# Performance work log

Measured on AMD Instinct MI355X. Metric: run time of the kernel, lower is better.

The kernel has to match this reference:

```python
import jax, jax.numpy as jnp
import numpy as np

KNOTS = 16
BOUND = 5.0
BATCH = 500000
X_DIM = 6          # split into lower(3) / upper(3)
C_DIM = 4
HID = 128
SPLINE_DIM = 3 * KNOTS - 1   # 47 (non-periodic)
LOWER = X_DIM // 2
OUT_DIM = LOWER * SPLINE_DIM


def setup_inputs() -> dict:
    key = jax.random.key(0)
    ks = jax.random.split(key, 10)
    def glorot(k, shape):
        fan_in, fan_out = shape
        s = jnp.sqrt(2.0 / (fan_in + fan_out))
        return (jax.random.normal(k, shape, jnp.float32) * s)
    return {
        "x": jax.random.normal(ks[0], (BATCH, X_DIM), jnp.float32),
        "c": jax.random.normal(ks[1], (BATCH, C_DIM), jnp.float32),
        "W1": glorot(ks[2], (LOWER + C_DIM + 0 + (X_DIM - LOWER), HID))[: X_DIM - LOWER + C_DIM],
        "b1": jnp.zeros((HID,), jnp.float32),
        "W2": glorot(ks[3], (HID, HID)),
        "b2": jnp.zeros((HID,), jnp.float32),
        "W3": glorot(ks[4], (HID, OUT_DIM)),
        "b3": jnp.zeros((OUT_DIM,), jnp.float32),
        "train": False,
    }


def _mlp(h, W1, b1, W2, b2, W3, b3):
    h = jax.nn.relu(h @ W1 + b1)
    h = jax.nn.relu(h @ W2 + b2)
    return h @ W3 + b3


def _rqs_forward(x, W, H, D, B):
    """Rational-quadratic spline (Durkan et al.) forward.
    x: [N,d]; W,H: [N,d,K] bin widths/heights; D: [N,d,K-1] interior derivs."""
    K = W.shape[-1]
    pad = jnp.full(W.shape[:-1] + (1,), -B, W.dtype)
    xk = jnp.concatenate([pad, -B + jnp.cumsum(W, axis=-1)], axis=-1)  # [N,d,K+1]
    yk = jnp.concatenate([pad, -B + jnp.cumsum(H, axis=-1)], axis=-1)
    one = jnp.ones(D.shape[:-1] + (1,), D.dtype)
    dk = jnp.concatenate([one, D, one], axis=-1)                        # [N,d,K+1]

    oob = (x <= -B) | (x >= B)
    xm = jnp.where(oob, -B, x)
    # bin index per element (searchsorted via comparison-sum)
    idx = jnp.clip(jnp.sum((xm[..., None] >= xk), axis=-1) - 1, 0, K - 1)[..., None]

    gat = lambda a, i: jnp.take_along_axis(a, i, axis=-1)[..., 0]
    xk_b = gat(xk, idx)
    yk_b = gat(yk, idx)
    wk = gat(xk, idx + 1) - xk_b
    hk = gat(yk, idx + 1) - yk_b
    dk_b = gat(dk, idx)
    dk1 = gat(dk, idx + 1)

    sk = hk / wk
    relx = jnp.clip((xm - xk_b) / wk, 0.0, 1.0)
    r1 = relx * (1.0 - relx)
    den = sk + (dk1 + dk_b - 2.0 * sk) * r1
    num = hk * (sk * relx * relx + dk_b * r1)
    y = yk_b + num / den
    ld = (2.0 * jnp.log(sk)
          + jnp.log(dk1 * relx * relx + 2.0 * sk * r1 + dk_b * (1.0 - relx) ** 2)
          - 2.0 * jnp.log(den))

    y = jnp.where(oob, x, y)
    ld = jnp.where(oob, 0.0, ld)
    return y, jnp.sum(ld, axis=1)


def reference(x, c, W1, b1, W2, b2, W3, b3, train):
    lower, upper = x[:, :LOWER], x[:, LOWER:]
    h = jnp.hstack((upper, c))
    p = _mlp(h, W1, b1, W2, b2, W3, b3)
    p = p.reshape(-1, LOWER, SPLINE_DIM)
    Wb, Hb, Db = jnp.split(p, [KNOTS, 2 * KNOTS], axis=2)
    Wb = 2.0 * BOUND * jax.nn.softmax(Wb, axis=-1)
    Hb = 2.0 * BOUND * jax.nn.softmax(Hb, axis=-1)
    Db = jax.nn.softplus(Db)
    lo_t, log_det = _rqs_forward(lower, Wb, Hb, Db, BOUND)
    y = jnp.hstack((lo_t, upper))
    return y, log_det
```

## Files before the change

### kernel.cpp

```cpp
#include <hip/hip_runtime.h>
#include <math.h>


#define TILE 128
#define NT   256
#define HID  128
#define OUTD 141
#define HS   136
#define PRS  48
#define SRS  152
#define BND  5.0f
#define T1   0.5413248546f

typedef __bf16 bf16;
typedef _Float16 f16;
typedef __attribute__((ext_vector_type(8))) __bf16 bf16x8;
typedef __attribute__((ext_vector_type(8))) _Float16 f16x8;
typedef __attribute__((ext_vector_type(4))) float f32x4;

#define W1P_ELEMS (8 * 64 * 8)
#define W2P_ELEMS (8 * 4 * 64 * 8)
#define W3P_ELEMS (9 * 4 * 64 * 8)

#define SMEM_BYTES 40448

__global__ void nsc_prepack(const float* __restrict__ W1, const float* __restrict__ W2,
                            const float* __restrict__ W3,
                            bf16* __restrict__ W1p, bf16* __restrict__ W2p,
                            bf16* __restrict__ W3p) {
    int f = blockIdx.x * 256 + threadIdx.x;
    int lane = f & 63, lm = lane & 15, lq = lane >> 4;
    if (f < 512) {
        int t = f >> 6;
        int n = t * 16 + lm;
        bf16x8 pk;
        #pragma unroll
        for (int j = 0; j < 8; ++j) {
            int k = lq * 8 + j;
            pk[j] = (k < 7) ? (bf16)W1[k * HID + n] : (bf16)0.f;
        }
        *(bf16x8*)&W1p[(size_t)f * 8] = pk;
    } else if (f < 512 + 2048) {
        int g2 = f - 512;
        int tk = g2 >> 6, t = tk >> 2, ks = tk & 3;
        int n = t * 16 + lm;
        bf16x8 pk;
        #pragma unroll
        for (int j = 0; j < 8; ++j) {
            int p = ks * 32 + lq * 8 + j;
            int k = ((p & 7) << 4) | (p >> 3);
            pk[j] = (bf16)W2[k * HID + n];
        }
        *(bf16x8*)&W2p[(size_t)g2 * 8] = pk;
    } else if (f < 512 + 2048 + 2304) {
        int g3 = f - 2560;
        int tk = g3 >> 6, t = tk >> 2, ks = tk & 3;
        int col = t * 16 + lm;
        bf16x8 pk;
        #pragma unroll
        for (int j = 0; j < 8; ++j) {
            int p = ks * 32 + lq * 8 + j;
            int k = ((p & 7) << 4) | (p >> 3);
            pk[j] = (col < OUTD) ? (bf16)W3[k * OUTD + col] : (bf16)0.f;
        }
        *(bf16x8*)&W3p[(size_t)g3 * 8] = pk;
    }
}

__global__ __launch_bounds__(NT, 4) void nsc_main(
    const float* __restrict__ x, const float* __restrict__ c,
    const bf16* __restrict__ W1p, const float* __restrict__ b1,
    const bf16* __restrict__ W2p, const float* __restrict__ b2,
    const bf16* __restrict__ W3p, const float* __restrict__ b3,
    float* __restrict__ out_y, float* __restrict__ out_ld, int N)
{
    __shared__ __align__(16) char smem[SMEM_BYTES];
    bf16*  hbuf  = (bf16*)smem;
    f16*   shp16 = (f16*)smem;
    float* shld  = (float*)(smem + 38912);

    const int tid  = threadIdx.x;
    const int g0   = blockIdx.x * TILE;
    const int lane = tid & 63;
    const int wv   = tid >> 6;
    const int lm   = lane & 15;
    const int lq   = lane >> 4;
    const int sbase = wv * 32;
    const int arow0 = sbase + lm;
    const int arow1 = sbase + 16 + lm;

    if (lane < 32) {
        int s = sbase + lane;
        int g = g0 + s;
        float v[7];
        if (g < N) {
            v[0] = x[g * 6 + 3]; v[1] = x[g * 6 + 4]; v[2] = x[g * 6 + 5];
            v[3] = c[g * 4];     v[4] = c[g * 4 + 1];
            v[5] = c[g * 4 + 2]; v[6] = c[g * 4 + 3];
        } else {
            #pragma unroll
            for (int k = 0; k < 7; ++k) v[k] = 0.f;
        }
        bf16x8 r0 = (bf16x8){(bf16)v[0], (bf16)v[1], (bf16)v[2], (bf16)v[3],
                             (bf16)v[4], (bf16)v[5], (bf16)v[6], (bf16)0.f};
        bf16x8 z  = (bf16x8){(bf16)0.f, (bf16)0.f, (bf16)0.f, (bf16)0.f,
                             (bf16)0.f, (bf16)0.f, (bf16)0.f, (bf16)0.f};
        *(bf16x8*)&hbuf[s * HS]      = r0;
        *(bf16x8*)&hbuf[s * HS + 8]  = z;
        *(bf16x8*)&hbuf[s * HS + 16] = z;
        *(bf16x8*)&hbuf[s * HS + 24] = z;
    }

    {
        f32x4 acc1[2][8];
        #pragma unroll
        for (int t = 0; t < 8; ++t) {
            float b = b1[t * 16 + lm];
            acc1[0][t] = (f32x4){b, b, b, b};
            acc1[1][t] = (f32x4){b, b, b, b};
        }
        bf16x8 a0 = *(const bf16x8*)&hbuf[arow0 * HS + lq * 8];
        bf16x8 a1 = *(const bf16x8*)&hbuf[arow1 * HS + lq * 8];
        #pragma unroll
        for (int t = 0; t < 8; ++t) {
            bf16x8 bf = *(const bf16x8*)&W1p[(size_t)(t * 64 + lane) * 8];
            acc1[0][t] = __builtin_amdgcn_mfma_f32_16x16x32_bf16(a0, bf, acc1[0][t], 0, 0, 0);
            acc1[1][t] = __builtin_amdgcn_mfma_f32_16x16x32_bf16(a1, bf, acc1[1][t], 0, 0, 0);
        }
        #pragma unroll
        for (int ar = 0; ar < 2; ++ar)
            #pragma unroll
            for (int r = 0; r < 4; ++r) {
                bf16x8 pk;
                #pragma unroll
                for (int t = 0; t < 8; ++t) pk[t] = (bf16)fmaxf(acc1[ar][t][r], 0.f);
                int s = sbase + ar * 16 + lq * 4 + r;
                *(bf16x8*)&hbuf[s * HS + lm * 8] = pk;
            }
    }

    {
        f32x4 acc2[2][8];
        #pragma unroll
        for (int t = 0; t < 8; ++t) {
            float b = b2[t * 16 + lm];
            acc2[0][t] = (f32x4){b, b, b, b};
            acc2[1][t] = (f32x4){b, b, b, b};
        }
        #pragma unroll
        for (int ks = 0; ks < 4; ++ks) {
            bf16x8 a0 = *(const bf16x8*)&hbuf[arow0 * HS + ks * 32 + lq * 8];
            bf16x8 a1 = *(const bf16x8*)&hbuf[arow1 * HS + ks * 32 + lq * 8];
            #pragma unroll
            for (int t = 0; t < 8; ++t) {
                bf16x8 bf = *(const bf16x8*)&W2p[(size_t)((t * 4 + ks) * 64 + lane) * 8];
                acc2[0][t] = __builtin_amdgcn_mfma_f32_16x16x32_bf16(a0, bf, acc2[0][t], 0, 0, 0);
                acc2[1][t] = __builtin_amdgcn_mfma_f32_16x16x32_bf16(a1, bf, acc2[1][t], 0, 0, 0);
            }
        }
        #pragma unroll
        for (int ar = 0; ar < 2; ++ar)
            #pragma unroll
            for (int r = 0; r < 4; ++r) {
                bf16x8 pk;
                #pragma unroll
                for (int t = 0; t < 8; ++t) pk[t] = (bf16)fmaxf(acc2[ar][t][r], 0.f);
                int s = sbase + ar * 16 + lq * 4 + r;
                *(bf16x8*)&hbuf[s * HS + lm * 8] = pk;
            }
    }

    f32x4 acc3[2][9];
    {
        #pragma unroll
        for (int t = 0; t < 9; ++t) {
            int col = t * 16 + lm;
            float b = (col < OUTD) ? b3[col] : 0.f;
            acc3[0][t] = (f32x4){b, b, b, b};
            acc3[1][t] = (f32x4){b, b, b, b};
        }
        #pragma unroll
        for (int ks = 0; ks < 4; ++ks) {
            bf16x8 a0 = *(const bf16x8*)&hbuf[arow0 * HS + ks * 32 + lq * 8];
            bf16x8 a1 = *(const bf16x8*)&hbuf[arow1 * HS + ks * 32 + lq * 8];
            #pragma unroll
            for (int t = 0; t < 9; ++t) {
                bf16x8 bf = *(const bf16x8*)&W3p[(size_t)((t * 4 + ks) * 64 + lane) * 8];
                acc3[0][t] = __builtin_amdgcn_mfma_f32_16x16x32_bf16(a0, bf, acc3[0][t], 0, 0, 0);
                acc3[1][t] = __builtin_amdgcn_mfma_f32_16x16x32_bf16(a1, bf, acc3[1][t], 0, 0, 0);
            }
        }
    }
    __syncthreads();

    #pragma unroll
    for (int t = 0; t < 9; ++t) {
        int col = t * 16 + lm;
        if (col < OUTD) {
            int d = (col >= 94) ? 2 : ((col >= 47) ? 1 : 0);
            int off = d * PRS + (col - d * 47);
            #pragma unroll
            for (int ar = 0; ar < 2; ++ar)
                #pragma unroll
                for (int r = 0; r < 4; ++r) {
                    int s = sbase + ar * 16 + lq * 4 + r;
                    shp16[s * SRS + off] = (f16)acc3[ar][t][r];
                }
        }
    }
    __syncthreads();

    for (int pidx = tid; pidx < TILE * 3; pidx += NT) {
        const int s = pidx / 3, d = pidx - s * 3;
        const int g = g0 + s;
        if (g < N) {
            const f16* pr = &shp16[s * SRS + d * PRS];
            f16x8 v0 = *(const f16x8*)&pr[0];
            f16x8 v1 = *(const f16x8*)&pr[8];
            f16x8 v2 = *(const f16x8*)&pr[16];
            f16x8 v3 = *(const f16x8*)&pr[24];
            f16x8 v4 = *(const f16x8*)&pr[32];
            f16x8 v5 = *(const f16x8*)&pr[40];
            float wv_[16], hv[16], dl[15];
            #pragma unroll
            for (int i = 0; i < 8; ++i) {
                wv_[i] = (float)v0[i]; wv_[8 + i] = (float)v1[i];
                hv[i]  = (float)v2[i]; hv[8 + i]  = (float)v3[i];
            }
            #pragma unroll
            for (int i = 0; i < 8; ++i) dl[i] = (float)v4[i];
            #pragma unroll
            for (int i = 0; i < 7; ++i) dl[8 + i] = (float)v5[i];

            float sw = 0.f, sh = 0.f;
            #pragma unroll
            for (int i = 0; i < 16; ++i) { wv_[i] = __expf(wv_[i]); sw += wv_[i]; }
            #pragma unroll
            for (int i = 0; i < 16; ++i) { hv[i]  = __expf(hv[i]);  sh += hv[i]; }
            float cwn = 10.f * __builtin_amdgcn_rcpf(sw);
            float chn = 10.f * __builtin_amdgcn_rcpf(sh);
            #pragma unroll
            for (int i = 0; i < 16; ++i) { wv_[i] *= cwn; hv[i] *= chn; }

            float xv = x[g * 6 + d];
            bool oob = (xv <= -BND) || (xv >= BND);
            float xm = oob ? -BND : xv;

            float cumx = -BND + wv_[0], cumy = -BND + hv[0];
            float xk_b = -BND, yk_b = -BND;
            float wk = wv_[0], hk = hv[0];
            float d0l = T1, d1l = dl[0];
            #pragma unroll
            for (int i = 1; i < 16; ++i) {
                bool ge = (xm >= cumx);
                if (ge) {
                    xk_b = cumx; yk_b = cumy;
                    wk = wv_[i]; hk = hv[i];
                    d0l = dl[i - 1];
                    d1l = (i < 15) ? dl[i] : T1;
                }
                cumx += wv_[i]; cumy += hv[i];
            }
            float d0 = (d0l > 15.f) ? d0l : __logf(1.f + __expf(d0l));
            float d1 = (d1l > 15.f) ? d1l : __logf(1.f + __expf(d1l));

            float rwk = __builtin_amdgcn_rcpf(wk);
            float sk = hk * rwk;
            float relx = (xm - xk_b) * rwk;
            relx = fminf(fmaxf(relx, 0.f), 1.f);
            float r1 = relx * (1.f - relx);
            float den = sk + (d1 + d0 - 2.f * sk) * r1;
            float iden = __builtin_amdgcn_rcpf(den);
            float num = hk * (sk * relx * relx + d0 * r1);
            float y = yk_b + num * iden;
            float omr = 1.f - relx;
            float arg = d1 * relx * relx + 2.f * sk * r1 + d0 * omr * omr;
            float ratio = sk * iden;
            float ld = __logf(ratio * ratio * arg);
            if (oob) { y = xv; ld = 0.f; }

            out_y[g * 6 + d] = y;
            out_y[g * 6 + 3 + d] = x[g * 6 + 3 + d];
            shld[s * 3 + d] = ld;
        }
    }
    __syncthreads();

    if (tid < TILE) {
        int g = g0 + tid;
        if (g < N)
            out_ld[g] = shld[tid * 3] + shld[tid * 3 + 1] + shld[tid * 3 + 2];
    }
}

extern "C" void kernel_launch(void* const* d_in, const int* in_sizes, int n_in,
                              void* d_out, int out_size, void* d_ws, size_t ws_size,
                              hipStream_t stream) {
    const float* x  = (const float*)d_in[0];
    const float* c  = (const float*)d_in[1];
    const float* W1 = (const float*)d_in[2];
    const float* b1 = (const float*)d_in[3];
    const float* W2 = (const float*)d_in[4];
    const float* b2 = (const float*)d_in[5];
    const float* W3 = (const float*)d_in[6];
    const float* b3 = (const float*)d_in[7];

    const int N = in_sizes[0] / 6;
    float* out_y  = (float*)d_out;
    float* out_ld = (float*)d_out + (size_t)N * 6;

    bf16* W1p = (bf16*)d_ws;
    bf16* W2p = W1p + W1P_ELEMS;
    bf16* W3p = W2p + W2P_ELEMS;

    int nfrag = 512 + 2048 + 2304;
    nsc_prepack<<<(nfrag + 255) / 256, 256, 0, stream>>>(W1, W2, W3, W1p, W2p, W3p);

    int nblocks = (N + TILE - 1) / TILE;
    nsc_main<<<nblocks, NT, 0, stream>>>(x, c, W1p, b1, W2p, b2, W3p, b3,
                                         out_y, out_ld, N);
}
```

Baseline: 159.1 us.

## Keep MLP activations in registers via transposed MFMA operand layout

Swaps the MFMA operand roles so the weights act as the A operand and the activations as B, with W2/W3 prepacked in a permuted feature order. The accumulator layout of one layer then feeds the next layer directly from registers, which removes the LDS round trips and syncs between MLP layers. Layer 2 and 3 are tiled so fewer accumulators are live at once, layer-3 outputs are written to LDS as packed f16x4 at contiguous offsets, and the spline stage assigns each wave one dimension with per-dimension unpacking. This adds register pressure from holding activation fragments and makes the spline loads unaligned for dimensions 1 and 2.

```diff
diff --git a/kernel.cpp b/kernel.cpp
--- a/kernel.cpp
+++ b/kernel.cpp
@@ -6,8 +6,6 @@
 #define NT   256
 #define HID  128
 #define OUTD 141
-#define HS   136
-#define PRS  48
 #define SRS  152
 #define BND  5.0f
 #define T1   0.5413248546f
@@ -16,54 +14,59 @@
 typedef _Float16 f16;
 typedef __attribute__((ext_vector_type(8))) __bf16 bf16x8;
 typedef __attribute__((ext_vector_type(8))) _Float16 f16x8;
+typedef __attribute__((ext_vector_type(4))) _Float16 f16x4;
+typedef __attribute__((ext_vector_type(2))) _Float16 f16x2;
 typedef __attribute__((ext_vector_type(4))) float f32x4;
 
 #define W1P_ELEMS (8 * 64 * 8)
 #define W2P_ELEMS (8 * 4 * 64 * 8)
 #define W3P_ELEMS (9 * 4 * 64 * 8)
+#define NFRAG (512 + 2048 + 2304)
+#define B3P_OFF ((W1P_ELEMS + W2P_ELEMS + W3P_ELEMS) * 2)
 
 #define SMEM_BYTES 40448
 
 __global__ void nsc_prepack(const float* __restrict__ W1, const float* __restrict__ W2,
-                            const float* __restrict__ W3,
+                            const float* __restrict__ W3, const float* __restrict__ b3,
                             bf16* __restrict__ W1p, bf16* __restrict__ W2p,
-                            bf16* __restrict__ W3p) {
+                            bf16* __restrict__ W3p, float* __restrict__ b3p) {
     int f = blockIdx.x * 256 + threadIdx.x;
     int lane = f & 63, lm = lane & 15, lq = lane >> 4;
     if (f < 512) {
         int t = f >> 6;
-        int n = t * 16 + lm;
+        int m = t * 16 + lm;
         bf16x8 pk;
         #pragma unroll
         for (int j = 0; j < 8; ++j) {
             int k = lq * 8 + j;
-            pk[j] = (k < 7) ? (bf16)W1[k * HID + n] : (bf16)0.f;
+            pk[j] = (k < 7) ? (bf16)W1[k * HID + m] : (bf16)0.f;
         }
         *(bf16x8*)&W1p[(size_t)f * 8] = pk;
     } else if (f < 512 + 2048) {
         int g2 = f - 512;
-        int tk = g2 >> 6, t = tk >> 2, ks = tk & 3;
-        int n = t * 16 + lm;
+        int tk = g2 >> 6, t2 = tk >> 2, kc = tk & 3;
+        int m = t2 * 16 + lm;
         bf16x8 pk;
         #pragma unroll
         for (int j = 0; j < 8; ++j) {
-            int p = ks * 32 + lq * 8 + j;
-            int k = ((p & 7) << 4) | (p >> 3);
-            pk[j] = (bf16)W2[k * HID + n];
+            int feat = ((kc * 2 + (j >> 2)) << 4) + (lq << 2) + (j & 3);
+            pk[j] = (bf16)W2[feat * HID + m];
         }
         *(bf16x8*)&W2p[(size_t)g2 * 8] = pk;
-    } else if (f < 512 + 2048 + 2304) {
+    } else if (f < NFRAG) {
         int g3 = f - 2560;
-        int tk = g3 >> 6, t = tk >> 2, ks = tk & 3;
-        int col = t * 16 + lm;
+        int tk = g3 >> 6, t3 = tk >> 2, kc = tk & 3;
+        int col = t3 * 16 + lm;
         bf16x8 pk;
         #pragma unroll
         for (int j = 0; j < 8; ++j) {
-            int p = ks * 32 + lq * 8 + j;
-            int k = ((p & 7) << 4) | (p >> 3);
-            pk[j] = (col < OUTD) ? (bf16)W3[k * OUTD + col] : (bf16)0.f;
+            int feat = ((kc * 2 + (j >> 2)) << 4) + (lq << 2) + (j & 3);
+            pk[j] = (col < OUTD) ? (bf16)W3[feat * OUTD + col] : (bf16)0.f;
         }
         *(bf16x8*)&W3p[(size_t)g3 * 8] = pk;
+    } else if (f < NFRAG + 144) {
+        int i = f - NFRAG;
+        b3p[i] = (i < OUTD) ? b3[i] : 0.f;
     }
 }
 
@@ -71,11 +74,10 @@
     const float* __restrict__ x, const float* __restrict__ c,
     const bf16* __restrict__ W1p, const float* __restrict__ b1,
     const bf16* __restrict__ W2p, const float* __restrict__ b2,
-    const bf16* __restrict__ W3p, const float* __restrict__ b3,
+    const bf16* __restrict__ W3p, const float* __restrict__ b3p,
     float* __restrict__ out_y, float* __restrict__ out_ld, int N)
 {
     __shared__ __align__(16) char smem[SMEM_BYTES];
-    bf16*  hbuf  = (bf16*)smem;
     f16*   shp16 = (f16*)smem;
     float* shld  = (float*)(smem + 38912);
 
@@ -86,180 +88,194 @@
     const int lm   = lane & 15;
     const int lq   = lane >> 4;
     const int sbase = wv * 32;
-    const int arow0 = sbase + lm;
-    const int arow1 = sbase + 16 + lm;
-
-    if (lane < 32) {
-        int s = sbase + lane;
-        int g = g0 + s;
-        float v[7];
-        if (g < N) {
+
+    bf16x8 inb[2];
+    #pragma unroll
+    for (int set = 0; set < 2; ++set) {
+        int g = g0 + sbase + set * 16 + lm;
+        float v[8] = {0.f, 0.f, 0.f, 0.f, 0.f, 0.f, 0.f, 0.f};
+        if (lq == 0 && g < N) {
             v[0] = x[g * 6 + 3]; v[1] = x[g * 6 + 4]; v[2] = x[g * 6 + 5];
             v[3] = c[g * 4];     v[4] = c[g * 4 + 1];
             v[5] = c[g * 4 + 2]; v[6] = c[g * 4 + 3];
-        } else {
-            #pragma unroll
-            for (int k = 0; k < 7; ++k) v[k] = 0.f;
-        }
-        bf16x8 r0 = (bf16x8){(bf16)v[0], (bf16)v[1], (bf16)v[2], (bf16)v[3],
-                             (bf16)v[4], (bf16)v[5], (bf16)v[6], (bf16)0.f};
-        bf16x8 z  = (bf16x8){(bf16)0.f, (bf16)0.f, (bf16)0.f, (bf16)0.f,
-                             (bf16)0.f, (bf16)0.f, (bf16)0.f, (bf16)0.f};
-        *(bf16x8*)&hbuf[s * HS]      = r0;
-        *(bf16x8*)&hbuf[s * HS + 8]  = z;
-        *(bf16x8*)&hbuf[s * HS + 16] = z;
-        *(bf16x8*)&hbuf[s * HS + 24] = z;
-    }
-
+        }
+        bf16x8 t;
+        #pragma unroll
+        for (int j = 0; j < 8; ++j) t[j] = (bf16)v[j];
+        inb[set] = t;
+    }
+
+    f32x4 acc1[2][8];
     {
-        f32x4 acc1[2][8];
         #pragma unroll
         for (int t = 0; t < 8; ++t) {
-            float b = b1[t * 16 + lm];
-            acc1[0][t] = (f32x4){b, b, b, b};
-            acc1[1][t] = (f32x4){b, b, b, b};
-        }
-        bf16x8 a0 = *(const bf16x8*)&hbuf[arow0 * HS + lq * 8];
-        bf16x8 a1 = *(const bf16x8*)&hbuf[arow1 * HS + lq * 8];
+            f32x4 bb = *(const f32x4*)&b1[t * 16 + lq * 4];
+            acc1[0][t] = bb; acc1[1][t] = bb;
+        }
         #pragma unroll
         for (int t = 0; t < 8; ++t) {
-            bf16x8 bf = *(const bf16x8*)&W1p[(size_t)(t * 64 + lane) * 8];
-            acc1[0][t] = __builtin_amdgcn_mfma_f32_16x16x32_bf16(a0, bf, acc1[0][t], 0, 0, 0);
-            acc1[1][t] = __builtin_amdgcn_mfma_f32_16x16x32_bf16(a1, bf, acc1[1][t], 0, 0, 0);
-        }
-        #pragma unroll
-        for (int ar = 0; ar < 2; ++ar)
-            #pragma unroll
-            for (int r = 0; r < 4; ++r) {
-                bf16x8 pk;
-                #pragma unroll
-                for (int t = 0; t < 8; ++t) pk[t] = (bf16)fmaxf(acc1[ar][t][r], 0.f);
-                int s = sbase + ar * 16 + lq * 4 + r;
-                *(bf16x8*)&hbuf[s * HS + lm * 8] = pk;
+            bf16x8 wf = *(const bf16x8*)&W1p[(size_t)(t * 64 + lane) * 8];
+            acc1[0][t] = __builtin_amdgcn_mfma_f32_16x16x32_bf16(wf, inb[0], acc1[0][t], 0, 0, 0);
+            acc1[1][t] = __builtin_amdgcn_mfma_f32_16x16x32_bf16(wf, inb[1], acc1[1][t], 0, 0, 0);
+        }
+    }
+    bf16x8 h1B[2][4];
+    #pragma unroll
+    for (int set = 0; set < 2; ++set)
+        #pragma unroll
+        for (int kc = 0; kc < 4; ++kc) {
+            bf16x8 hb;
+            #pragma unroll
+            for (int j = 0; j < 8; ++j)
+                hb[j] = (bf16)fmaxf(acc1[set][kc * 2 + (j >> 2)][j & 3], 0.f);
+            h1B[set][kc] = hb;
+        }
+
+    bf16x8 h2B[2][4];
+    #pragma unroll
+    for (int tp = 0; tp < 4; ++tp) {
+        f32x4 acc[2][2];
+        #pragma unroll
+        for (int dt = 0; dt < 2; ++dt) {
+            f32x4 bb = *(const f32x4*)&b2[(tp * 2 + dt) * 16 + lq * 4];
+            acc[0][dt] = bb; acc[1][dt] = bb;
+        }
+        #pragma unroll
+        for (int kc = 0; kc < 4; ++kc)
+            #pragma unroll
+            for (int dt = 0; dt < 2; ++dt) {
+                bf16x8 wf = *(const bf16x8*)&W2p[(size_t)(((tp * 2 + dt) * 4 + kc) * 64 + lane) * 8];
+                acc[0][dt] = __builtin_amdgcn_mfma_f32_16x16x32_bf16(wf, h1B[0][kc], acc[0][dt], 0, 0, 0);
+                acc[1][dt] = __builtin_amdgcn_mfma_f32_16x16x32_bf16(wf, h1B[1][kc], acc[1][dt], 0, 0, 0);
             }
-    }
-
-    {
-        f32x4 acc2[2][8];
-        #pragma unroll
-        for (int t = 0; t < 8; ++t) {
-            float b = b2[t * 16 + lm];
-            acc2[0][t] = (f32x4){b, b, b, b};
-            acc2[1][t] = (f32x4){b, b, b, b};
-        }
-        #pragma unroll
-        for (int ks = 0; ks < 4; ++ks) {
-            bf16x8 a0 = *(const bf16x8*)&hbuf[arow0 * HS + ks * 32 + lq * 8];
-            bf16x8 a1 = *(const bf16x8*)&hbuf[arow1 * HS + ks * 32 + lq * 8];
-            #pragma unroll
-            for (int t = 0; t < 8; ++t) {
-                bf16x8 bf = *(const bf16x8*)&W2p[(size_t)((t * 4 + ks) * 64 + lane) * 8];
-                acc2[0][t] = __builtin_amdgcn_mfma_f32_16x16x32_bf16(a0, bf, acc2[0][t], 0, 0, 0);
-                acc2[1][t] = __builtin_amdgcn_mfma_f32_16x16x32_bf16(a1, bf, acc2[1][t], 0, 0, 0);
+        #pragma unroll
+        for (int set = 0; set < 2; ++set) {
+            bf16x8 hb;
+            #pragma unroll
+            for (int j = 0; j < 8; ++j)
+                hb[j] = (bf16)fmaxf(acc[set][j >> 2][j & 3], 0.f);
+            h2B[set][tp] = hb;
+        }
+    }
+
+    #pragma unroll
+    for (int t3 = 0; t3 < 9; ++t3) {
+        f32x4 acc[2];
+        {
+            f32x4 bb = *(const f32x4*)&b3p[t3 * 16 + lq * 4];
+            acc[0] = bb; acc[1] = bb;
+        }
+        #pragma unroll
+        for (int kc = 0; kc < 4; ++kc) {
+            bf16x8 wf = *(const bf16x8*)&W3p[(size_t)((t3 * 4 + kc) * 64 + lane) * 8];
+            acc[0] = __builtin_amdgcn_mfma_f32_16x16x32_bf16(wf, h2B[0][kc], acc[0], 0, 0, 0);
+            acc[1] = __builtin_amdgcn_mfma_f32_16x16x32_bf16(wf, h2B[1][kc], acc[1], 0, 0, 0);
+        }
+        #pragma unroll
+        for (int set = 0; set < 2; ++set) {
+            int s = sbase + set * 16 + lm;
+            f16x4 pk = (f16x4){(f16)acc[set][0], (f16)acc[set][1],
+                               (f16)acc[set][2], (f16)acc[set][3]};
+            int off = t3 * 16 + lq * 4;
+            if (t3 < 8) {
+                *(f16x4*)&shp16[s * SRS + off] = pk;
+            } else {
+                if (lq < 3) *(f16x4*)&shp16[s * SRS + off] = pk;
+                else        shp16[s * SRS + 140] = pk[0];
             }
         }
-        #pragma unroll
-        for (int ar = 0; ar < 2; ++ar)
-            #pragma unroll
-            for (int r = 0; r < 4; ++r) {
-                bf16x8 pk;
-                #pragma unroll
-                for (int t = 0; t < 8; ++t) pk[t] = (bf16)fmaxf(acc2[ar][t][r], 0.f);
-                int s = sbase + ar * 16 + lq * 4 + r;
-                *(bf16x8*)&hbuf[s * HS + lm * 8] = pk;
-            }
-    }
-
-    f32x4 acc3[2][9];
-    {
-        #pragma unroll
-        for (int t = 0; t < 9; ++t) {
-            int col = t * 16 + lm;
-            float b = (col < OUTD) ? b3[col] : 0.f;
-            acc3[0][t] = (f32x4){b, b, b, b};
-            acc3[1][t] = (f32x4){b, b, b, b};
-        }
-        #pragma unroll
-        for (int ks = 0; ks < 4; ++ks) {
-            bf16x8 a0 = *(const bf16x8*)&hbuf[arow0 * HS + ks * 32 + lq * 8];
-            bf16x8 a1 = *(const bf16x8*)&hbuf[arow1 * HS + ks * 32 + lq * 8];
-            #pragma unroll
-            for (int t = 0; t < 9; ++t) {
-                bf16x8 bf = *(const bf16x8*)&W3p[(size_t)((t * 4 + ks) * 64 + lane) * 8];
-                acc3[0][t] = __builtin_amdgcn_mfma_f32_16x16x32_bf16(a0, bf, acc3[0][t], 0, 0, 0);
-                acc3[1][t] = __builtin_amdgcn_mfma_f32_16x16x32_bf16(a1, bf, acc3[1][t], 0, 0, 0);
-            }
-        }
     }
     __syncthreads();
 
-    #pragma unroll
-    for (int t = 0; t < 9; ++t) {
-        int col = t * 16 + lm;
-        if (col < OUTD) {
-            int d = (col >= 94) ? 2 : ((col >= 47) ? 1 : 0);
-            int off = d * PRS + (col - d * 47);
-            #pragma unroll
-            for (int ar = 0; ar < 2; ++ar)
-                #pragma unroll
-                for (int r = 0; r < 4; ++r) {
-                    int s = sbase + ar * 16 + lq * 4 + r;
-                    shp16[s * SRS + off] = (f16)acc3[ar][t][r];
-                }
-        }
-    }
-    __syncthreads();
-
-    for (int pidx = tid; pidx < TILE * 3; pidx += NT) {
-        const int s = pidx / 3, d = pidx - s * 3;
+    for (int grp = wv; grp < 6; grp += 4) {
+        const int d = grp >> 1;
+        const int s = ((grp & 1) << 6) + lane;
         const int g = g0 + s;
         if (g < N) {
-            const f16* pr = &shp16[s * SRS + d * PRS];
-            f16x8 v0 = *(const f16x8*)&pr[0];
-            f16x8 v1 = *(const f16x8*)&pr[8];
-            f16x8 v2 = *(const f16x8*)&pr[16];
-            f16x8 v3 = *(const f16x8*)&pr[24];
-            f16x8 v4 = *(const f16x8*)&pr[32];
-            f16x8 v5 = *(const f16x8*)&pr[40];
-            float wv_[16], hv[16], dl[15];
-            #pragma unroll
-            for (int i = 0; i < 8; ++i) {
-                wv_[i] = (float)v0[i]; wv_[8 + i] = (float)v1[i];
-                hv[i]  = (float)v2[i]; hv[8 + i]  = (float)v3[i];
+            const f16* pr = &shp16[s * SRS];
+            float w_[16], h_[16], dl[15];
+            if (d == 0) {
+                f16x8 A0 = *(const f16x8*)&pr[0],  A1 = *(const f16x8*)&pr[8];
+                f16x8 A2 = *(const f16x8*)&pr[16], A3 = *(const f16x8*)&pr[24];
+                f16x8 A4 = *(const f16x8*)&pr[32], A5 = *(const f16x8*)&pr[40];
+                #pragma unroll
+                for (int i = 0; i < 8; ++i) {
+                    w_[i] = (float)A0[i]; w_[8 + i] = (float)A1[i];
+                    h_[i] = (float)A2[i]; h_[8 + i] = (float)A3[i];
+                    dl[i] = (float)A4[i];
+                }
+                #pragma unroll
+                for (int i = 0; i < 7; ++i) dl[8 + i] = (float)A5[i];
+            } else if (d == 1) {
+                float a47 = (float)pr[47];
+                f16x8 A0 = *(const f16x8*)&pr[48], A1 = *(const f16x8*)&pr[56];
+                f16x8 A2 = *(const f16x8*)&pr[64], A3 = *(const f16x8*)&pr[72];
+                f16x8 A4 = *(const f16x8*)&pr[80], A5 = *(const f16x8*)&pr[88];
+                w_[0] = a47;
+                #pragma unroll
+                for (int i = 0; i < 8; ++i) w_[1 + i] = (float)A0[i];
+                #pragma unroll
+                for (int i = 0; i < 7; ++i) w_[9 + i] = (float)A1[i];
+                h_[0] = (float)A1[7];
+                #pragma unroll
+                for (int i = 0; i < 8; ++i) h_[1 + i] = (float)A2[i];
+                #pragma unroll
+                for (int i = 0; i < 7; ++i) h_[9 + i] = (float)A3[i];
+                dl[0] = (float)A3[7];
+                #pragma unroll
+                for (int i = 0; i < 8; ++i) dl[1 + i] = (float)A4[i];
+                #pragma unroll
+                for (int i = 0; i < 6; ++i) dl[9 + i] = (float)A5[i];
+            } else {
+                f16x2 B  = *(const f16x2*)&pr[94];
+                f16x8 C0 = *(const f16x8*)&pr[96],  C1 = *(const f16x8*)&pr[104];
+                f16x8 C2 = *(const f16x8*)&pr[112], C3 = *(const f16x8*)&pr[120];
+                f16x8 C4 = *(const f16x8*)&pr[128], E  = *(const f16x8*)&pr[136];
+                w_[0] = (float)B[0]; w_[1] = (float)B[1];
+                #pragma unroll
+                for (int i = 0; i < 8; ++i) w_[2 + i] = (float)C0[i];
+                #pragma unroll
+                for (int i = 0; i < 6; ++i) w_[10 + i] = (float)C1[i];
+                h_[0] = (float)C1[6]; h_[1] = (float)C1[7];
+                #pragma unroll
+                for (int i = 0; i < 8; ++i) h_[2 + i] = (float)C2[i];
+                #pragma unroll
+                for (int i = 0; i < 6; ++i) h_[10 + i] = (float)C3[i];
+                dl[0] = (float)C3[6]; dl[1] = (float)C3[7];
+                #pragma unroll
+                for (int i = 0; i < 8; ++i) dl[2 + i] = (float)C4[i];
+                #pragma unroll
+                for (int i = 0; i < 5; ++i) dl[10 + i] = (float)E[i];
             }
-            #pragma unroll
-            for (int i = 0; i < 8; ++i) dl[i] = (float)v4[i];
-            #pragma unroll
-            for (int i = 0; i < 7; ++i) dl[8 + i] = (float)v5[i];
 
             float sw = 0.f, sh = 0.f;
             #pragma unroll
-            for (int i = 0; i < 16; ++i) { wv_[i] = __expf(wv_[i]); sw += wv_[i]; }
-            #pragma unroll
-            for (int i = 0; i < 16; ++i) { hv[i]  = __expf(hv[i]);  sh += hv[i]; }
+            for (int i = 0; i < 16; ++i) { w_[i] = __expf(w_[i]); sw += w_[i]; }
+            #pragma unroll
+            for (int i = 0; i < 16; ++i) { h_[i] = __expf(h_[i]); sh += h_[i]; }
             float cwn = 10.f * __builtin_amdgcn_rcpf(sw);
             float chn = 10.f * __builtin_amdgcn_rcpf(sh);
             #pragma unroll
-            for (int i = 0; i < 16; ++i) { wv_[i] *= cwn; hv[i] *= chn; }
+            for (int i = 0; i < 16; ++i) { w_[i] *= cwn; h_[i] *= chn; }
 
             float xv = x[g * 6 + d];
             bool oob = (xv <= -BND) || (xv >= BND);
             float xm = oob ? -BND : xv;
 
-            float cumx = -BND + wv_[0], cumy = -BND + hv[0];
+            float cumx = -BND + w_[0], cumy = -BND + h_[0];
             float xk_b = -BND, yk_b = -BND;
-            float wk = wv_[0], hk = hv[0];
+            float wk = w_[0], hk = h_[0];
             float d0l = T1, d1l = dl[0];
             #pragma unroll
             for (int i = 1; i < 16; ++i) {
                 bool ge = (xm >= cumx);
                 if (ge) {
                     xk_b = cumx; yk_b = cumy;
-                    wk = wv_[i]; hk = hv[i];
+                    wk = w_[i]; hk = h_[i];
                     d0l = dl[i - 1];
                     d1l = (i < 15) ? dl[i] : T1;
                 }
-                cumx += wv_[i]; cumy += hv[i];
+                cumx += w_[i]; cumy += h_[i];
             }
             float d0 = (d0l > 15.f) ? d0l : __logf(1.f + __expf(d0l));
             float d1 = (d1l > 15.f) ? d1l : __logf(1.f + __expf(d1l));
@@ -309,14 +325,16 @@
     float* out_y  = (float*)d_out;
     float* out_ld = (float*)d_out + (size_t)N * 6;
 
-    bf16* W1p = (bf16*)d_ws;
-    bf16* W2p = W1p + W1P_ELEMS;
-    bf16* W3p = W2p + W2P_ELEMS;
-
-    int nfrag = 512 + 2048 + 2304;
-    nsc_prepack<<<(nfrag + 255) / 256, 256, 0, stream>>>(W1, W2, W3, W1p, W2p, W3p);
+    bf16*  W1p = (bf16*)d_ws;
+    bf16*  W2p = W1p + W1P_ELEMS;
+    bf16*  W3p = W2p + W2P_ELEMS;
+    float* b3p = (float*)((char*)d_ws + B3P_OFF);
+
+    int nthreads = NFRAG + 144;
+    nsc_prepack<<<(nthreads + 255) / 256, 256, 0, stream>>>(W1, W2, W3, b3,
+                                                            W1p, W2p, W3p, b3p);
 
     int nblocks = (N + TILE - 1) / TILE;
-    nsc_main<<<nblocks, NT, 0, stream>>>(x, c, W1p, b1, W2p, b2, W3p, b3,
+    nsc_main<<<nblocks, NT, 0, stream>>>(x, c, W1p, b1, W2p, b2, W3p, b3p,
                                          out_y, out_ld, N);
 }
```

Result: no change. 161.4 us (+1.4%).
